# Performance work log

Measured on AMD Instinct MI355X. Metric: run time of the kernel, lower is better.

## Reference

```python
import jax, jax.numpy as jnp
import numpy as np

NUM_HEADS = 16
NEG_INF = -1000000.0  # matches torch masked_fill value


def setup_inputs() -> dict:
    key = jax.random.key(0)
    k1, k2, k3, k4, k5, k6 = jax.random.split(key, 6)
    N, S, E = 2, 2048, 1024
    x_encoder = jax.random.normal(k1, (N, S, E), dtype=jnp.float32)
    x_decoder = jax.random.normal(k2, (N, S, E), dtype=jnp.float32)
    mask = jax.random.randint(k3, (S, S), 0, 2, dtype=jnp.int32)
    W_qk = jax.random.normal(k4, (2 * E, E), dtype=jnp.float32) * (1.0 / np.sqrt(E))
    W_v = jax.random.normal(k5, (E, E), dtype=jnp.float32) * (1.0 / np.sqrt(E))
    W_o = jax.random.normal(k6, (E, E), dtype=jnp.float32) * (1.0 / np.sqrt(E))
    return {"x_encoder": x_encoder, "x_decoder": x_decoder, "mask": mask,
            "W_qk": W_qk, "W_v": W_v, "W_o": W_o}


def reference(x_encoder, x_decoder, mask, W_qk, W_v, W_o):
    N, S, E = x_encoder.shape
    H = NUM_HEADS
    hd = E // H
    # projections (no bias)
    qk = x_encoder @ W_qk.T            # (N, S, 2E)
    v = x_decoder @ W_v.T              # (N, S, E)
    qk = qk.reshape(N, S, H, 2 * hd).transpose(0, 2, 1, 3)  # (N, H, S, 2hd)
    v = v.reshape(N, S, H, hd).transpose(0, 2, 1, 3)         # (N, H, S, hd)
    q, k = qk[..., :hd], qk[..., hd:]
    # scaled dot-product attention with mask fill
    logits = jnp.einsum('bhqd,bhkd->bhqk', q, k) / jnp.sqrt(jnp.float32(hd))
    m = mask[None, None, :, :]  # expand_mask: 2D -> (1,1,S,S)
    logits = jnp.where(m == 0, jnp.float32(NEG_INF), logits)
    attn = jax.nn.softmax(logits, axis=-1)
    vals = jnp.einsum('bhqk,bhkd->bhqd', attn, v)            # (N, H, S, hd)
    vals = vals.transpose(0, 2, 1, 3).reshape(N, S, E)
    return vals @ W_o.T
```

## Files before the change

### kernel.cpp

```cpp
#include <hip/hip_runtime.h>

typedef __attribute__((ext_vector_type(8))) short short8;
typedef __attribute__((ext_vector_type(4))) float f32x4;
typedef __attribute__((ext_vector_type(4))) unsigned short u16x4;
typedef __attribute__((ext_vector_type(4))) unsigned int u32x4;

#define MFMA16(A,B,C) __builtin_amdgcn_mfma_f32_16x16x32_bf16(A,B,C,0,0,0)

__device__ __forceinline__ unsigned short f2bf(float f) {
  unsigned int u = __builtin_bit_cast(unsigned int, f);
  unsigned int r = (u + 0x7fffu + ((u >> 16) & 1u)) >> 16;
  return (unsigned short)r;
}

__device__ __forceinline__ unsigned int cvt_pk_bf16(float lo, float hi) {
  unsigned int r;
  asm("v_cvt_pk_bf16_f32 %0, %1, %2" : "=v"(r) : "v"(lo), "v"(hi));
  return r;
}

__device__ __forceinline__ f32x4 zero4() {
  f32x4 z; z.x = 0.f; z.y = 0.f; z.z = 0.f; z.w = 0.f; return z;
}

__device__ __forceinline__ void gl_lds16(const void* g, void* l) {
  __builtin_amdgcn_global_load_lds((const __attribute__((address_space(1))) void*)g,
                                   (__attribute__((address_space(3))) void*)l, 16, 0, 0);
}

__global__ __launch_bounds__(256) void prep(const float* __restrict__ xe,
                                            const float* __restrict__ xd,
                                            const float* __restrict__ wqk,
                                            const float* __restrict__ wv,
                                            const float* __restrict__ wo,
                                            const int* __restrict__ mask,
                                            unsigned int* __restrict__ mbits,
                                            unsigned short* __restrict__ ws) {
  if (blockIdx.x >= 12288) {
    int idx = (blockIdx.x - 12288) * 256 + threadIdx.x;
    int row = idx >> 6, wi = idx & 63;
    const int* p = mask + (long)row * 2048 + wi * 32;
    unsigned int bits = 0;
    #pragma unroll
    for (int j = 0; j < 32; j++) bits |= (p[j] != 0 ? 1u : 0u) << j;
    mbits[idx] = bits;
    return;
  }
  long i = (long)blockIdx.x * 256 + threadIdx.x;
  const float* src; unsigned short* dst; long o; bool scl = false;
  if (i < 1048576)      { src = xe;  dst = ws + 8650752;  o = i; }
  else if (i < 2097152) { src = xd;  dst = ws + 12845056; o = i - 1048576; }
  else if (i < 2621440) { src = wqk; dst = ws + 17039360; o = i - 2097152;
                          scl = (((o >> 8) & 127) < 64); }
  else if (i < 2883584) { src = wv;  dst = ws + 19136512; o = i - 2621440; }
  else                  { src = wo;  dst = ws + 20185088; o = i - 2883584; }
  float4 f = ((const float4*)src)[o];
  if (scl) {
    const float SCQ = 0.125f * 1.4426950408889634f;
    f.x *= SCQ; f.y *= SCQ; f.z *= SCQ; f.w *= SCQ;
  }
  u16x4 r; r.x = f2bf(f.x); r.y = f2bf(f.y); r.z = f2bf(f.z); r.w = f2bf(f.w);
  ((u16x4*)dst)[o] = r;
}

__global__ __launch_bounds__(256) void gemm_qkv(const unsigned short* __restrict__ xe,
                                                const unsigned short* __restrict__ xd,
                                                const unsigned short* __restrict__ wqk,
                                                const unsigned short* __restrict__ wv,
                                                unsigned short* __restrict__ qkb,
                                                unsigned short* __restrict__ vTb) {
  __shared__ __align__(16) unsigned short As[128 * 64];
  __shared__ __align__(16) unsigned short Bs[128 * 64];
  const int bid = blockIdx.x;
  const unsigned short* A; const unsigned short* B;
  long row0, col0; int mode;
  if (bid < 512) { A = xe; B = wqk; row0 = (long)(bid >> 4) * 128; col0 = (long)(bid & 15) * 128; mode = 0; }
  else { int id = bid - 512; A = xd; B = wv; row0 = (long)(id >> 3) * 128; col0 = (long)(id & 7) * 128; mode = 1; }

  const int tid = threadIdx.x;
  const int w = tid >> 6, l = tid & 63;
  const int wr = w >> 1, wc = w & 1;
  const int lr = l >> 3;
  const int lc = (l & 7) * 8;

  f32x4 acc[4][4];
  #pragma unroll
  for (int m = 0; m < 4; m++)
    #pragma unroll
    for (int n = 0; n < 4; n++) acc[m][n] = zero4();

  for (int k0 = 0; k0 < 1024; k0 += 64) {
    #pragma unroll
    for (int j = 0; j < 4; j++) {
      int slot = j * 4 + w;
      int row = slot * 8 + lr;
      gl_lds16(A + (row0 + row) * 1024 + k0 + lc, &As[slot * 512]);
      gl_lds16(B + (col0 + row) * 1024 + k0 + lc, &Bs[slot * 512]);
    }
    __syncthreads();
    #pragma unroll
    for (int kk = 0; kk < 2; kk++) {
      short8 a[4], b[4];
      #pragma unroll
      for (int m = 0; m < 4; m++)
        a[m] = *(const short8*)&As[(wr * 64 + m * 16 + (l & 15)) * 64 + kk * 32 + (l >> 4) * 8];
      #pragma unroll
      for (int n = 0; n < 4; n++)
        b[n] = *(const short8*)&Bs[(wc * 64 + n * 16 + (l & 15)) * 64 + kk * 32 + (l >> 4) * 8];
      #pragma unroll
      for (int m = 0; m < 4; m++)
        #pragma unroll
        for (int n = 0; n < 4; n++)
          acc[m][n] = MFMA16(a[m], b[n], acc[m][n]);
    }
    __syncthreads();
  }

  #pragma unroll
  for (int m = 0; m < 4; m++) {
    long rowb = row0 + wr * 64 + m * 16 + ((l >> 4) * 4);
    #pragma unroll
    for (int n = 0; n < 4; n++) {
      long colb = col0 + wc * 64 + n * 16 + (l & 15);
      if (mode == 0) {
        #pragma unroll
        for (int r = 0; r < 4; r++) qkb[(rowb + r) * 2048 + colb] = f2bf(acc[m][n][r]);
      } else {
        long bb = rowb >> 11, s0 = rowb & 2047;
        u16x4 pk;
        pk.x = f2bf(acc[m][n][0]); pk.y = f2bf(acc[m][n][1]);
        pk.z = f2bf(acc[m][n][2]); pk.w = f2bf(acc[m][n][3]);
        *(u16x4*)&vTb[(bb * 1024 + colb) * 2048 + s0] = pk;
      }
    }
  }
}

__global__ __launch_bounds__(256) void gemm_out(const unsigned short* __restrict__ A,
                                                const unsigned short* __restrict__ B,
                                                float* __restrict__ C) {
  __shared__ __align__(16) unsigned short As[128 * 64];
  __shared__ __align__(16) unsigned short Bs[64 * 64];
  const int tid = threadIdx.x;
  const int w = tid >> 6, l = tid & 63;
  const int wr = w >> 1, wc = w & 1;
  const long row0 = (long)blockIdx.y * 128;
  const long col0 = (long)blockIdx.x * 64;
  const int lr = l >> 3;
  const int lc = (l & 7) * 8;

  f32x4 acc[4][2];
  #pragma unroll
  for (int m = 0; m < 4; m++)
    #pragma unroll
    for (int n = 0; n < 2; n++) acc[m][n] = zero4();

  for (int k0 = 0; k0 < 1024; k0 += 64) {
    #pragma unroll
    for (int j = 0; j < 4; j++) {
      int slot = j * 4 + w;
      int row = slot * 8 + lr;
      gl_lds16(A + (row0 + row) * 1024 + k0 + lc, &As[slot * 512]);
    }
    #pragma unroll
    for (int j = 0; j < 2; j++) {
      int slot = j * 4 + w;
      int row = slot * 8 + lr;
      gl_lds16(B + (col0 + row) * 1024 + k0 + lc, &Bs[slot * 512]);
    }
    __syncthreads();
    #pragma unroll
    for (int kk = 0; kk < 2; kk++) {
      short8 a[4], b[2];
      #pragma unroll
      for (int m = 0; m < 4; m++)
        a[m] = *(const short8*)&As[(wr * 64 + m * 16 + (l & 15)) * 64 + kk * 32 + (l >> 4) * 8];
      #pragma unroll
      for (int n = 0; n < 2; n++)
        b[n] = *(const short8*)&Bs[(wc * 32 + n * 16 + (l & 15)) * 64 + kk * 32 + (l >> 4) * 8];
      #pragma unroll
      for (int m = 0; m < 4; m++)
        #pragma unroll
        for (int n = 0; n < 2; n++)
          acc[m][n] = MFMA16(a[m], b[n], acc[m][n]);
    }
    __syncthreads();
  }

  #pragma unroll
  for (int m = 0; m < 4; m++) {
    long rowb = row0 + wr * 64 + m * 16 + ((l >> 4) * 4);
    #pragma unroll
    for (int n = 0; n < 2; n++) {
      long colb = col0 + wc * 32 + n * 16 + (l & 15);
      #pragma unroll
      for (int r = 0; r < 4; r++) C[(rowb + r) * 1024 + colb] = acc[m][n][r];
    }
  }
}

__device__ __forceinline__ void softmax_pack(const f32x4* sf, unsigned long long mw,
                                             int g, int sA, int sB, int gh,
                                             float& l_run, short8& pa0o, short8& pa1o) {
  mw >>= (g * 4);
  unsigned int mlo = (unsigned int)mw, mhi = (unsigned int)(mw >> 32);
  float pv[16];
  float lsum = 0.f;
  #pragma unroll
  for (int kvq = 0; kvq < 4; kvq++) {
    unsigned int msel = (kvq < 2) ? mlo : mhi;
    #pragma unroll
    for (int r = 0; r < 4; r++) {
      float e = __builtin_amdgcn_exp2f(sf[kvq][r]);
      unsigned int bit = (msel >> (((kvq & 1) << 4) + r)) & 1u;
      float p = bit ? e : 0.0f;
      pv[kvq * 4 + r] = p;
      lsum += p;
    }
  }
  l_run += lsum;

  unsigned int pk0[2], pk1[2], pk2[2], pk3[2];
  pk0[0] = cvt_pk_bf16(pv[0],  pv[1]);  pk0[1] = cvt_pk_bf16(pv[2],  pv[3]);
  pk1[0] = cvt_pk_bf16(pv[4],  pv[5]);  pk1[1] = cvt_pk_bf16(pv[6],  pv[7]);
  pk2[0] = cvt_pk_bf16(pv[8],  pv[9]);  pk2[1] = cvt_pk_bf16(pv[10], pv[11]);
  pk3[0] = cvt_pk_bf16(pv[12], pv[13]); pk3[1] = cvt_pk_bf16(pv[14], pv[15]);

  u32x4 a0, a1;
  int t0, t1;
  t0 = __shfl((int)pk0[0], sA); t1 = __shfl((int)pk1[0], sA);
  a0.x = gh ? (unsigned)t1 : (unsigned)t0;
  t0 = __shfl((int)pk0[1], sA); t1 = __shfl((int)pk1[1], sA);
  a0.y = gh ? (unsigned)t1 : (unsigned)t0;
  t0 = __shfl((int)pk0[0], sB); t1 = __shfl((int)pk1[0], sB);
  a0.z = gh ? (unsigned)t1 : (unsigned)t0;
  t0 = __shfl((int)pk0[1], sB); t1 = __shfl((int)pk1[1], sB);
  a0.w = gh ? (unsigned)t1 : (unsigned)t0;
  t0 = __shfl((int)pk2[0], sA); t1 = __shfl((int)pk3[0], sA);
  a1.x = gh ? (unsigned)t1 : (unsigned)t0;
  t0 = __shfl((int)pk2[1], sA); t1 = __shfl((int)pk3[1], sA);
  a1.y = gh ? (unsigned)t1 : (unsigned)t0;
  t0 = __shfl((int)pk2[0], sB); t1 = __shfl((int)pk3[0], sB);
  a1.z = gh ? (unsigned)t1 : (unsigned)t0;
  t0 = __shfl((int)pk2[1], sB); t1 = __shfl((int)pk3[1], sB);
  a1.w = gh ? (unsigned)t1 : (unsigned)t0;
  pa0o = __builtin_bit_cast(short8, a0);
  pa1o = __builtin_bit_cast(short8, a1);
}

__global__ __launch_bounds__(256, 4) void attn(const unsigned short* __restrict__ qk,
                                               const unsigned short* __restrict__ vT,
                                               const unsigned int* __restrict__ mbits,
                                               unsigned short* __restrict__ po0,
                                               unsigned short* __restrict__ po1,
                                               unsigned short* __restrict__ po2,
                                               unsigned short* __restrict__ po3,
                                               float* __restrict__ pl0,
                                               float* __restrict__ pl1,
                                               float* __restrict__ pl2,
                                               float* __restrict__ pl3) {
  __shared__ __align__(16) unsigned short Ks[2][64 * 64];
  __shared__ __align__(16) unsigned short Vs[2][64 * 64];
  const int tid = threadIdx.x;
  const int w = tid >> 6, l = tid & 63;
  const int b = blockIdx.z, h = blockIdx.y;
  const int qt = blockIdx.x & 15, kvh = blockIdx.x >> 4;
  const int q0 = qt * 128;
  const int kvbase = kvh << 9;
  unsigned short* po = (kvh == 0) ? po0 : (kvh == 1) ? po1 : (kvh == 2) ? po2 : po3;
  float* pl = (kvh == 0) ? pl0 : (kvh == 1) ? pl1 : (kvh == 2) ? pl2 : pl3;
  const int c = l & 15, g = l >> 4;
  const int lr = l >> 3, pg = l & 7;

  const int qa = q0 + w * 32 + c;
  const int qb = qa + 16;
  const unsigned short* qptrA = qk + (long)(b * 2048 + qa) * 2048 + h * 128;
  const unsigned short* qptrB = qk + (long)(b * 2048 + qb) * 2048 + h * 128;
  short8 bqA0 = *(const short8*)&qptrA[g * 8];
  short8 bqA1 = *(const short8*)&qptrA[32 + g * 8];
  short8 bqB0 = *(const short8*)&qptrB[g * 8];
  short8 bqB1 = *(const short8*)&qptrB[32 + g * 8];

  const int sw0 = ((g)     ^ (c & 7)) * 8;
  const int sw1 = ((g + 4) ^ (c & 7)) * 8;
  const int sA = c + (((2 * g)     & 3) << 4);
  const int sB = c + (((2 * g + 1) & 3) << 4);
  const int gh = g >> 1;

  const unsigned int* mwordA = mbits + (long)qa * 64 + (kvbase >> 5);
  const unsigned int* mwordB = mbits + (long)qb * 64 + (kvbase >> 5);
  u32x4 mAw[4], mBw[4];
  #pragma unroll
  for (int j = 0; j < 4; j++) {
    mAw[j] = *(const u32x4*)&mwordA[j * 4];
    mBw[j] = *(const u32x4*)&mwordB[j * 4];
  }

  const unsigned short* kbase = qk + (long)b * 2048 * 2048 + h * 128 + 64;
  const unsigned short* vbase = vT + (long)((b * 16 + h) * 64) * 2048;
  const int srow = w * 8 + lr;
  const int sgg = pg ^ (lr & 7);

  float lA = 0.f, lB = 0.f;
  f32x4 oA[4], oB[4];
  #pragma unroll
  for (int d = 0; d < 4; d++) { oA[d] = zero4(); oB[d] = zero4(); }

  #pragma unroll
  for (int j = 0; j < 2; j++) {
    int row = srow + j * 32;
    gl_lds16(kbase + (long)(kvbase + row) * 2048 + sgg * 8, &Ks[0][(w + j * 4) * 512]);
    gl_lds16(vbase + (long)row * 2048 + kvbase + sgg * 8,   &Vs[0][(w + j * 4) * 512]);
  }
  __syncthreads();

  #pragma unroll
  for (int it = 0; it < 8; it++) {
    const int kv0 = kvbase + it * 64;
    const int cur = it & 1;

    if (it < 7) {
      #pragma unroll
      for (int j = 0; j < 2; j++) {
        int row = srow + j * 32;
        gl_lds16(kbase + (long)(kv0 + 64 + row) * 2048 + sgg * 8,
                 &Ks[cur ^ 1][(w + j * 4) * 512]);
        gl_lds16(vbase + (long)row * 2048 + kv0 + 64 + sgg * 8,
                 &Vs[cur ^ 1][(w + j * 4) * 512]);
      }
    }

    unsigned long long mwA = ((unsigned long long)mAw[it >> 1][(2 * it + 1) & 3] << 32)
                           | mAw[it >> 1][(2 * it) & 3];
    unsigned long long mwB = ((unsigned long long)mBw[it >> 1][(2 * it + 1) & 3] << 32)
                           | mBw[it >> 1][(2 * it) & 3];

    f32x4 sfA[4], sfB[4];
    __builtin_amdgcn_s_setprio(1);
    #pragma unroll
    for (int kvq = 0; kvq < 4; kvq++) {
      int R = kvq * 16 + c;
      short8 ak0 = *(const short8*)&Ks[cur][R * 64 + sw0];
      short8 ak1 = *(const short8*)&Ks[cur][R * 64 + sw1];
      f32x4 zA = zero4();
      zA = MFMA16(ak0, bqA0, zA);
      zA = MFMA16(ak1, bqA1, zA);
      sfA[kvq] = zA;
      f32x4 zB = zero4();
      zB = MFMA16(ak0, bqB0, zB);
      zB = MFMA16(ak1, bqB1, zB);
      sfB[kvq] = zB;
    }
    __builtin_amdgcn_s_setprio(0);

    short8 paA0, paA1, paB0, paB1;
    softmax_pack(sfA, mwA, g, sA, sB, gh, lA, paA0, paA1);
    softmax_pack(sfB, mwB, g, sA, sB, gh, lB, paB0, paB1);

    __builtin_amdgcn_s_setprio(1);
    #pragma unroll
    for (int dt = 0; dt < 4; dt++) {
      int d = dt * 16 + c;
      short8 bv0 = *(const short8*)&Vs[cur][d * 64 + sw0];
      short8 bv1 = *(const short8*)&Vs[cur][d * 64 + sw1];
      oA[dt] = MFMA16(paA0, bv0, oA[dt]);
      oA[dt] = MFMA16(paA1, bv1, oA[dt]);
      oB[dt] = MFMA16(paB0, bv0, oB[dt]);
      oB[dt] = MFMA16(paB1, bv1, oB[dt]);
    }
    __builtin_amdgcn_s_setprio(0);

    __syncthreads();
  }

  lA += __shfl_xor(lA, 16); lA += __shfl_xor(lA, 32);
  lB += __shfl_xor(lB, 16); lB += __shfl_xor(lB, 32);
  if (g == 0) {
    pl[((long)(b << 11) + qa) * 16 + h] = lA;
    pl[((long)(b << 11) + qb) * 16 + h] = lB;
  }
  #pragma unroll
  for (int dt = 0; dt < 4; dt++) {
    long rowA = (long)b * 2048 + q0 + w * 32 + g * 4;
    long rowB = rowA + 16;
    int col = h * 64 + dt * 16 + c;
    po[(rowA + 0) * 1024 + col] = f2bf(oA[dt][0]);
    po[(rowA + 1) * 1024 + col] = f2bf(oA[dt][1]);
    po[(rowA + 2) * 1024 + col] = f2bf(oA[dt][2]);
    po[(rowA + 3) * 1024 + col] = f2bf(oA[dt][3]);
    po[(rowB + 0) * 1024 + col] = f2bf(oB[dt][0]);
    po[(rowB + 1) * 1024 + col] = f2bf(oB[dt][1]);
    po[(rowB + 2) * 1024 + col] = f2bf(oB[dt][2]);
    po[(rowB + 3) * 1024 + col] = f2bf(oB[dt][3]);
  }
}

__global__ __launch_bounds__(256) void combine(const unsigned short* __restrict__ po0,
                                               const unsigned short* __restrict__ po1,
                                               const unsigned short* __restrict__ po2,
                                               const unsigned short* __restrict__ po3,
                                               const float* __restrict__ pl0,
                                               const float* __restrict__ pl1,
                                               const float* __restrict__ pl2,
                                               const float* __restrict__ pl3,
                                               unsigned short* __restrict__ vals) {
  int i = blockIdx.x * 256 + threadIdx.x;
  int q = i >> 7;
  int col = (i & 127) * 8;
  int h = col >> 6;
  float linv = 1.0f / (pl0[q * 16 + h] + pl1[q * 16 + h] + pl2[q * 16 + h] + pl3[q * 16 + h]);
  long off = (long)q * 1024 + col;
  short8 a = *(const short8*)&po0[off];
  short8 b = *(const short8*)&po1[off];
  short8 cc = *(const short8*)&po2[off];
  short8 d = *(const short8*)&po3[off];
  short8 o;
  #pragma unroll
  for (int j = 0; j < 8; j++) {
    float fa = __builtin_bit_cast(float, ((unsigned int)(unsigned short)a[j]) << 16);
    float fb = __builtin_bit_cast(float, ((unsigned int)(unsigned short)b[j]) << 16);
    float fc = __builtin_bit_cast(float, ((unsigned int)(unsigned short)cc[j]) << 16);
    float fd = __builtin_bit_cast(float, ((unsigned int)(unsigned short)d[j]) << 16);
    o[j] = (short)f2bf((fa + fb + fc + fd) * linv);
  }
  *(short8*)&vals[off] = o;
}

extern "C" void kernel_launch(void* const* d_in, const int* in_sizes, int n_in,
                              void* d_out, int out_size, void* d_ws, size_t ws_size,
                              hipStream_t stream) {
  const float* xe  = (const float*)d_in[0];
  const float* xd  = (const float*)d_in[1];
  const int*   msk = (const int*)d_in[2];
  const float* wqk = (const float*)d_in[3];
  const float* wv  = (const float*)d_in[4];
  const float* wo  = (const float*)d_in[5];
  float* out = (float*)d_out;
  unsigned short* ws = (unsigned short*)d_ws;

  unsigned short* po0    = ws;
  unsigned short* po1    = ws + 4194304;
  float*          pl0    = (float*)(ws + 8388608);
  float*          pl1    = (float*)(ws + 8519680);
  unsigned short* xe_bf  = ws + 8650752;
  unsigned short* xd_bf  = ws + 12845056;
  unsigned short* wqk_bf = ws + 17039360;
  unsigned short* wv_bf  = ws + 19136512;
  unsigned short* wo_bf  = ws + 20185088;
  unsigned short* qkb    = ws + 21233664;
  unsigned short* vTb    = ws + 29622272;
  unsigned short* valb   = ws + 33816576;
  unsigned int*   mbits  = (unsigned int*)(ws + 38010880);
  unsigned short* po2    = xe_bf;
  unsigned short* po3    = xd_bf;
  float*          pl2    = (float*)wqk_bf;
  float*          pl3    = (float*)(wqk_bf + 131072);

  prep<<<12800, 256, 0, stream>>>(xe, xd, wqk, wv, wo, msk, mbits, ws);
  gemm_qkv<<<768, 256, 0, stream>>>(xe_bf, xd_bf, wqk_bf, wv_bf, qkb, vTb);
  attn<<<dim3(64, 16, 2), 256, 0, stream>>>(qkb, vTb, mbits,
                                            po0, po1, po2, po3, pl0, pl1, pl2, pl3);
  combine<<<2048, 256, 0, stream>>>(po0, po1, po2, po3, pl0, pl1, pl2, pl3, valb);
  gemm_out<<<dim3(16, 32), 256, 0, stream>>>(valb, wo_bf, out);
}
```

Before: 169.6 us.

## Remap block indices so each XCD works on contiguous tiles for L2 locality

Renumbers the blocks of the QKV GEMM, attention and output GEMM kernels so that blocks landing on the same XCD (bid & 7) share row tiles or the same (batch, head) group. This aims to raise L2 reuse of A rows and K/V tiles within each chiplet's private cache. The attention kernel also stops unrolling the KV loop, drops the s_setprio hints, and loads mask words per iteration from global memory instead of preloading them into registers. That lowers register pressure but adds a global load inside the loop.

```diff
diff --git a/kernel.cpp b/kernel.cpp
--- a/kernel.cpp
+++ b/kernel.cpp
@@ -74,8 +74,18 @@
   const int bid = blockIdx.x;
   const unsigned short* A; const unsigned short* B;
   long row0, col0; int mode;
-  if (bid < 512) { A = xe; B = wqk; row0 = (long)(bid >> 4) * 128; col0 = (long)(bid & 15) * 128; mode = 0; }
-  else { int id = bid - 512; A = xd; B = wv; row0 = (long)(id >> 3) * 128; col0 = (long)(id & 7) * 128; mode = 1; }
+  if (bid < 512) {
+    int xcd = bid & 7, j = bid >> 3;
+    A = xe; B = wqk; mode = 0;
+    row0 = (long)(xcd * 4 + (j >> 4)) * 128;
+    col0 = (long)(j & 15) * 128;
+  } else {
+    int p = bid - 512;
+    int xcd = p & 7, j = p >> 3;
+    A = xd; B = wv; mode = 1;
+    row0 = (long)(xcd * 4 + (j >> 3)) * 128;
+    col0 = (long)(j & 7) * 128;
+  }
 
   const int tid = threadIdx.x;
   const int w = tid >> 6, l = tid & 63;
@@ -141,11 +151,13 @@
                                                 float* __restrict__ C) {
   __shared__ __align__(16) unsigned short As[128 * 64];
   __shared__ __align__(16) unsigned short Bs[64 * 64];
+  const int i = blockIdx.x;
+  const int xcd = i & 7, j = i >> 3;
+  const long row0 = (long)(xcd * 4 + (j >> 4)) * 128;
+  const long col0 = (long)(j & 15) * 64;
   const int tid = threadIdx.x;
   const int w = tid >> 6, l = tid & 63;
   const int wr = w >> 1, wc = w & 1;
-  const long row0 = (long)blockIdx.y * 128;
-  const long col0 = (long)blockIdx.x * 64;
   const int lr = l >> 3;
   const int lc = (l & 7) * 8;
 
@@ -157,14 +169,14 @@
 
   for (int k0 = 0; k0 < 1024; k0 += 64) {
     #pragma unroll
-    for (int j = 0; j < 4; j++) {
-      int slot = j * 4 + w;
+    for (int jj = 0; jj < 4; jj++) {
+      int slot = jj * 4 + w;
       int row = slot * 8 + lr;
       gl_lds16(A + (row0 + row) * 1024 + k0 + lc, &As[slot * 512]);
     }
     #pragma unroll
-    for (int j = 0; j < 2; j++) {
-      int slot = j * 4 + w;
+    for (int jj = 0; jj < 2; jj++) {
+      int slot = jj * 4 + w;
       int row = slot * 8 + lr;
       gl_lds16(B + (col0 + row) * 1024 + k0 + lc, &Bs[slot * 512]);
     }
@@ -263,8 +275,13 @@
   __shared__ __align__(16) unsigned short Vs[2][64 * 64];
   const int tid = threadIdx.x;
   const int w = tid >> 6, l = tid & 63;
-  const int b = blockIdx.z, h = blockIdx.y;
-  const int qt = blockIdx.x & 15, kvh = blockIdx.x >> 4;
+  const int i = blockIdx.x;
+  const int xcd = i & 7, jj = i >> 3;
+  const int grp = xcd * 16 + (jj >> 4);
+  const int qt = jj & 15;
+  const int kvh = grp & 3;
+  const int h = (grp >> 2) & 15;
+  const int b = grp >> 6;
   const int q0 = qt * 128;
   const int kvbase = kvh << 9;
   unsigned short* po = (kvh == 0) ? po0 : (kvh == 1) ? po1 : (kvh == 2) ? po2 : po3;
@@ -287,14 +304,8 @@
   const int sB = c + (((2 * g + 1) & 3) << 4);
   const int gh = g >> 1;
 
-  const unsigned int* mwordA = mbits + (long)qa * 64 + (kvbase >> 5);
-  const unsigned int* mwordB = mbits + (long)qb * 64 + (kvbase >> 5);
-  u32x4 mAw[4], mBw[4];
-  #pragma unroll
-  for (int j = 0; j < 4; j++) {
-    mAw[j] = *(const u32x4*)&mwordA[j * 4];
-    mBw[j] = *(const u32x4*)&mwordB[j * 4];
-  }
+  const unsigned int* mrowA = mbits + (long)qa * 64;
+  const unsigned int* mrowB = mbits + (long)qb * 64;
 
   const unsigned short* kbase = qk + (long)b * 2048 * 2048 + h * 128 + 64;
   const unsigned short* vbase = vT + (long)((b * 16 + h) * 64) * 2048;
@@ -314,7 +325,6 @@
   }
   __syncthreads();
 
-  #pragma unroll
   for (int it = 0; it < 8; it++) {
     const int kv0 = kvbase + it * 64;
     const int cur = it & 1;
@@ -330,13 +340,10 @@
       }
     }
 
-    unsigned long long mwA = ((unsigned long long)mAw[it >> 1][(2 * it + 1) & 3] << 32)
-                           | mAw[it >> 1][(2 * it) & 3];
-    unsigned long long mwB = ((unsigned long long)mBw[it >> 1][(2 * it + 1) & 3] << 32)
-                           | mBw[it >> 1][(2 * it) & 3];
+    unsigned long long mwA = *(const unsigned long long*)&mrowA[kv0 >> 5];
+    unsigned long long mwB = *(const unsigned long long*)&mrowB[kv0 >> 5];
 
     f32x4 sfA[4], sfB[4];
-    __builtin_amdgcn_s_setprio(1);
     #pragma unroll
     for (int kvq = 0; kvq < 4; kvq++) {
       int R = kvq * 16 + c;
@@ -351,13 +358,11 @@
       zB = MFMA16(ak1, bqB1, zB);
       sfB[kvq] = zB;
     }
-    __builtin_amdgcn_s_setprio(0);
 
     short8 paA0, paA1, paB0, paB1;
     softmax_pack(sfA, mwA, g, sA, sB, gh, lA, paA0, paA1);
     softmax_pack(sfB, mwB, g, sA, sB, gh, lB, paB0, paB1);
 
-    __builtin_amdgcn_s_setprio(1);
     #pragma unroll
     for (int dt = 0; dt < 4; dt++) {
       int d = dt * 16 + c;
@@ -368,7 +373,6 @@
       oB[dt] = MFMA16(paB0, bv0, oB[dt]);
       oB[dt] = MFMA16(paB1, bv1, oB[dt]);
     }
-    __builtin_amdgcn_s_setprio(0);
 
     __syncthreads();
   }
@@ -458,8 +462,8 @@
 
   prep<<<12800, 256, 0, stream>>>(xe, xd, wqk, wv, wo, msk, mbits, ws);
   gemm_qkv<<<768, 256, 0, stream>>>(xe_bf, xd_bf, wqk_bf, wv_bf, qkb, vTb);
-  attn<<<dim3(64, 16, 2), 256, 0, stream>>>(qkb, vTb, mbits,
-                                            po0, po1, po2, po3, pl0, pl1, pl2, pl3);
+  attn<<<2048, 256, 0, stream>>>(qkb, vTb, mbits,
+                                 po0, po1, po2, po3, pl0, pl1, pl2, pl3);
   combine<<<2048, 256, 0, stream>>>(po0, po1, po2, po3, pl0, pl1, pl2, pl3, valb);
-  gemm_out<<<dim3(16, 32), 256, 0, stream>>>(valb, wo_bf, out);
-}
+  gemm_out<<<512, 256, 0, stream>>>(valb, wo_bf, out);
+}
```

After: 167.7 us. About the same (-1.1%).
